# Kernel optimization log

Measured on AMD Instinct MI355X. Metric: run time of the kernel, lower is better.

## Reference

```python
import jax, jax.numpy as jnp
import numpy as np

HEADS, LEVELS, POINTS, DIMS = 8, 4, 4, 256
CH = DIMS // HEADS
SHAPES = np.array([[96, 96], [48, 48], [24, 24], [12, 12]], dtype=np.int64)
LEVEL_START = np.concatenate([[0], np.cumsum(SHAPES[:, 0] * SHAPES[:, 1])[:-1]]).astype(np.int64)
HW = int((SHAPES[:, 0] * SHAPES[:, 1]).sum())
N, Q = 2, HW


def setup_inputs() -> dict:
    key = jax.random.key(0)
    ks = jax.random.split(key, 8)
    return {
        "q": jax.random.normal(ks[0], (N, Q, DIMS), jnp.float32),
        "p": jax.random.uniform(ks[1], (N, Q, LEVELS, 2), jnp.float32),
        "v": jax.random.normal(ks[2], (N, HW, DIMS), jnp.float32),
        "W_off": jax.random.normal(ks[3], (DIMS, HEADS * LEVELS * POINTS * 2), jnp.float32) * 0.01,
        "b_off": jax.random.normal(ks[4], (HEADS * LEVELS * POINTS * 2,), jnp.float32) * 0.5,
        "W_attn": jax.random.normal(ks[5], (DIMS, HEADS * LEVELS * POINTS), jnp.float32) * 0.02,
        "b_attn": jnp.zeros((HEADS * LEVELS * POINTS,), jnp.float32),
        "W_in": jax.random.normal(ks[6], (DIMS, DIMS), jnp.float32) / np.float32(np.sqrt(DIMS)),
        "b_in": jnp.zeros((DIMS,), jnp.float32),
        "W_out": jax.random.normal(ks[7], (DIMS, DIMS), jnp.float32) / np.float32(np.sqrt(DIMS)),
        "b_out": jnp.zeros((DIMS,), jnp.float32),
        "shapes": jnp.asarray(SHAPES),
        "level_index": jnp.asarray(LEVEL_START),
    }


def _sample_level(vl, loc_l, Hl, Wl):
    """Bilinear sample with zero padding outside the feature map.
    vl: [N, Hl*Wl, heads, C]; loc_l: [N, Q, heads, P, 2] normalized (x, y) in [0,1].
    Returns [N, Q, P, heads, C]."""
    Nb, Qn, Hd, P, _ = loc_l.shape
    x = loc_l[..., 0] * Wl - 0.5  # pixel coords, align_corners=False convention
    y = loc_l[..., 1] * Hl - 0.5
    x0 = jnp.floor(x)
    y0 = jnp.floor(y)
    dx = x - x0
    dy = y - y0
    x0i = x0.astype(jnp.int32)
    y0i = y0.astype(jnp.int32)
    out = jnp.zeros((Nb, Qn, P, Hd, vl.shape[-1]), vl.dtype)
    corners = ((x0i, y0i, (1 - dx) * (1 - dy)), (x0i + 1, y0i, dx * (1 - dy)),
               (x0i, y0i + 1, (1 - dx) * dy), (x0i + 1, y0i + 1, dx * dy))
    for cx, cy, w in corners:
        valid = (cx >= 0) & (cx < Wl) & (cy >= 0) & (cy < Hl)
        idx = jnp.clip(cy, 0, Hl - 1) * Wl + jnp.clip(cx, 0, Wl - 1)  # [N,Q,Hd,P]
        idx_t = idx.transpose(0, 1, 3, 2).reshape(Nb, Qn * P, Hd, 1)
        g = jnp.take_along_axis(vl, idx_t, axis=1).reshape(Nb, Qn, P, Hd, -1)
        wv = jnp.where(valid, w, 0.0).transpose(0, 1, 3, 2)  # [N,Q,P,Hd]
        out = out + g * wv[..., None].astype(vl.dtype)
    return out


def _forward(q, p, v, W_off, b_off, W_attn, b_attn, W_in, b_in, W_out, b_out, shp, lsi):
    Nb, Qn, _ = q.shape
    v = (v @ W_in + b_in).reshape(Nb, -1, HEADS, CH)
    off = (q @ W_off + b_off).reshape(Nb, Qn, HEADS, LEVELS, POINTS, 2)
    attn = jax.nn.softmax((q @ W_attn + b_attn).reshape(Nb, Qn, HEADS, LEVELS * POINTS), axis=-1)
    attn = attn.reshape(Nb, Qn, HEADS, LEVELS, POINTS)
    # offsets normalized by (W, H) of each level, added to reference points (2-coord branch)
    off_norm = jnp.asarray(np.stack([shp[:, 1], shp[:, 0]], -1), q.dtype)  # [L, 2]
    loc = p[:, :, None, :, None, :] + off / off_norm[None, None, None, :, None, :]  # [N,Q,Hd,L,P,2]
    out = jnp.zeros((Nb, Qn, HEADS, CH), q.dtype)
    for l in range(LEVELS):
        Hl, Wl = int(shp[l, 0]), int(shp[l, 1])
        s = int(lsi[l])
        vl = jax.lax.slice_in_dim(v, s, s + Hl * Wl, axis=1)
        samp = _sample_level(vl, loc[:, :, :, l], Hl, Wl)  # [N,Q,P,Hd,C]
        out = out + jnp.einsum('nqphc,nqhp->nqhc', samp, attn[:, :, :, l])
    return out.reshape(Nb, Qn, DIMS) @ W_out + b_out


def reference(q, p, v, W_off, b_off, W_attn, b_attn, W_in, b_in, W_out, b_out, shapes, level_index):
    shp = np.asarray(shapes)  # spatial shapes are structural constants
    lsi = np.asarray(level_index)
    return _forward(q, p, v, W_off, b_off, W_attn, b_attn, W_in, b_in, W_out, b_out, shp, lsi)
```

## Files before the change

kernel.cpp:

```cpp
#include <hip/hip_runtime.h>
#include <hip/hip_bf16.h>
#include <math.h>

#define NB      2
#define QN      12240
#define HW_TOT  12240
#define DIMS    256
#define HEADS   8
#define CH      32
#define LEVELS  4
#define POINTS  4
#define M_TOT   (NB * QN)

typedef unsigned short ushort_t;
typedef __attribute__((ext_vector_type(8))) short short8;
typedef __attribute__((ext_vector_type(4))) float floatx4;

__device__ __constant__ int c_Hl[4]    = {96, 48, 24, 12};
__device__ __constant__ int c_Wl[4]    = {96, 48, 24, 12};
__device__ __constant__ int c_start[4] = {0, 9216, 11520, 12096};

__device__ __forceinline__ ushort_t f2bf(float f) {
    __hip_bfloat16 h = __float2bfloat16(f);
    return *reinterpret_cast<ushort_t*>(&h);
}

__global__ __launch_bounds__(256) void convert_qv_kernel(
    const float* __restrict__ v, const float* __restrict__ q,
    ushort_t* __restrict__ vbf, ushort_t* __restrict__ qbf)
{
    const size_t i = ((size_t)blockIdx.x * 256 + threadIdx.x) * 8;
    const size_t half = (size_t)M_TOT * DIMS;
    const float* src; ushort_t* dst; size_t off;
    if (i < half) { src = v; dst = vbf; off = i; }
    else          { src = q; dst = qbf; off = i - half; }
    const float4 a = *(const float4*)&src[off];
    const float4 b = *(const float4*)&src[off + 4];
    ushort_t t[8] = {f2bf(a.x), f2bf(a.y), f2bf(a.z), f2bf(a.w),
                     f2bf(b.x), f2bf(b.y), f2bf(b.z), f2bf(b.w)};
    *(int4*)&dst[off] = *(int4*)t;
}

__global__ __launch_bounds__(256) void prep_weights_kernel(
    const float* __restrict__ W_in, const float* __restrict__ W_off,
    const float* __restrict__ W_attn, const float* __restrict__ W_out,
    const float* __restrict__ b_off, const float* __restrict__ b_attn,
    ushort_t* __restrict__ Tin, ushort_t* __restrict__ Tcomb,
    ushort_t* __restrict__ Tout, float* __restrict__ bcomb)
{
    const int z  = blockIdx.z;
    const int gi = blockIdx.x * 256 + threadIdx.x;
    if (z == 1 && gi < 384)
        bcomb[gi] = (gi < 256) ? b_off[gi] : b_attn[gi - 256];
    const int Nw = (z == 1) ? 384 : 256;
    if (gi >= Nw * 256) return;
    const int k = gi & 255;
    const int n = gi >> 8;
    float val; ushort_t* T;
    if (z == 0)      { val = W_in[k * 256 + n];  T = Tin;  }
    else if (z == 1) { val = (n < 256) ? W_off[k * 256 + n]
                                       : W_attn[k * 128 + (n - 256)]; T = Tcomb; }
    else             { val = W_out[k * 256 + n]; T = Tout; }
    T[n * 256 + k] = f2bf(val);
}

__device__ __forceinline__ void gemm_tile_core(
    const ushort_t* __restrict__ A, const ushort_t* __restrict__ BT,
    const float* __restrict__ bias, void* __restrict__ C, bool c_bf16,
    int M, int Nc, int bm0, int bn0, int K,
    ushort_t* As, ushort_t* Bs)
{
    const int tid  = threadIdx.x;
    const int wave = tid >> 6;
    const int lane = tid & 63;
    const int quad = lane >> 4;
    const int l16  = lane & 15;
    const int wm   = (wave >> 1) * 64;
    const int wn   = (wave & 1) * 64;

    const int off0 = tid * 16;
    const int row0 = off0 >> 6;
    const int kc0  = (off0 & 63) >> 1;

    int ar0 = bm0 + row0;      if (ar0 > M - 1) ar0 = M - 1;
    int ar1 = bm0 + row0 + 64; if (ar1 > M - 1) ar1 = M - 1;

    const ushort_t* ga0 = A  + (size_t)ar0 * K + kc0;
    const ushort_t* ga1 = A  + (size_t)ar1 * K + kc0;
    const ushort_t* gb0 = BT + (size_t)(bn0 + row0) * K + kc0;
    const ushort_t* gb1 = BT + (size_t)(bn0 + row0 + 64) * K + kc0;

    ushort_t* lA0 = As + wave * 512;
    ushort_t* lA1 = As + wave * 512 + 2048;
    ushort_t* lB0 = Bs + wave * 512;
    ushort_t* lB1 = Bs + wave * 512 + 2048;

    floatx4 acc[4][4];
    #pragma unroll
    for (int i = 0; i < 4; ++i)
        #pragma unroll
        for (int j = 0; j < 4; ++j)
            acc[i][j] = (floatx4){0.f, 0.f, 0.f, 0.f};

    for (int kk = 0; kk < K; kk += 32) {
        __builtin_amdgcn_global_load_lds(
            (const __attribute__((address_space(1))) void*)(ga0 + kk),
            (__attribute__((address_space(3))) void*)lA0, 16, 0, 0);
        __builtin_amdgcn_global_load_lds(
            (const __attribute__((address_space(1))) void*)(ga1 + kk),
            (__attribute__((address_space(3))) void*)lA1, 16, 0, 0);
        __builtin_amdgcn_global_load_lds(
            (const __attribute__((address_space(1))) void*)(gb0 + kk),
            (__attribute__((address_space(3))) void*)lB0, 16, 0, 0);
        __builtin_amdgcn_global_load_lds(
            (const __attribute__((address_space(1))) void*)(gb1 + kk),
            (__attribute__((address_space(3))) void*)lB1, 16, 0, 0);
        __syncthreads();

        short8 af[4], bfr[4];
        #pragma unroll
        for (int mt = 0; mt < 4; ++mt)
            af[mt] = *(const short8*)&As[(wm + mt * 16 + l16) * 32 + quad * 8];
        #pragma unroll
        for (int nt = 0; nt < 4; ++nt)
            bfr[nt] = *(const short8*)&Bs[(wn + nt * 16 + l16) * 32 + quad * 8];
        #pragma unroll
        for (int mt = 0; mt < 4; ++mt)
            #pragma unroll
            for (int nt = 0; nt < 4; ++nt)
                acc[mt][nt] = __builtin_amdgcn_mfma_f32_16x16x32_bf16(
                    af[mt], bfr[nt], acc[mt][nt], 0, 0, 0);
        __syncthreads();
    }

    #pragma unroll
    for (int mt = 0; mt < 4; ++mt) {
        #pragma unroll
        for (int j = 0; j < 4; ++j) {
            const int row = bm0 + wm + mt * 16 + quad * 4 + j;
            if (row >= M) continue;
            #pragma unroll
            for (int nt = 0; nt < 4; ++nt) {
                const int col = bn0 + wn + nt * 16 + l16;
                const float val = acc[mt][nt][j] + bias[col];
                if (c_bf16) ((ushort_t*)C)[(size_t)row * Nc + col] = f2bf(val);
                else        ((float*)C)[(size_t)row * Nc + col]    = val;
            }
        }
    }
}

__global__ __launch_bounds__(256) void gemm_proj_kernel(
    const ushort_t* __restrict__ vbf, const ushort_t* __restrict__ qbf,
    const ushort_t* __restrict__ Tin, const ushort_t* __restrict__ Tcomb,
    const float* __restrict__ b_in, const float* __restrict__ bcomb,
    ushort_t* __restrict__ vproj, float* __restrict__ offlog)
{
    __shared__ ushort_t As[128 * 32];
    __shared__ ushort_t Bs[128 * 32];
    const int bm0 = blockIdx.x * 128;
    const int y = blockIdx.y;
    if (y < 2)
        gemm_tile_core(vbf, Tin, b_in, vproj, true, M_TOT, 256, bm0, y * 128, 256, As, Bs);
    else
        gemm_tile_core(qbf, Tcomb, bcomb, offlog, false, M_TOT, 384, bm0, (y - 2) * 128, 256, As, Bs);
}

__global__ __launch_bounds__(256) void gemm_out_kernel(
    const ushort_t* __restrict__ mid, const ushort_t* __restrict__ Tout,
    const float* __restrict__ b_out, float* __restrict__ out)
{
    __shared__ ushort_t As[128 * 32];
    __shared__ ushort_t Bs[128 * 32];
    gemm_tile_core(mid, Tout, b_out, out, false, M_TOT, 256,
                   blockIdx.x * 128, blockIdx.y * 128, 256, As, Bs);
}

#define QB 2
#define SLOTS 576

__global__ __launch_bounds__(128) void msda_sample_kernel(
    const ushort_t* __restrict__ vproj, const float* __restrict__ offlog,
    const float* __restrict__ p, ushort_t* __restrict__ mid)
{
    __shared__ float s_logit[QB][128];
    __shared__ float s_off[QB][256];
    __shared__ float s_p[QB][8];
    __shared__ float s_mx[QB][HEADS];
    __shared__ float s_inv[QB][HEADS];
    __shared__ float s_w[QB][SLOTS];
    __shared__ int   s_idx[QB][SLOTS];

    const int tid = threadIdx.x;
    const int bq0 = blockIdx.x * QB;

    #pragma unroll
    for (int i = tid; i < QB * 256; i += 128) {
        int sub = i >> 8, j = i & 255;
        s_off[sub][j] = offlog[(size_t)(bq0 + sub) * 384 + j];
    }
    #pragma unroll
    for (int i = tid; i < QB * 128; i += 128) {
        int sub = i >> 7, j = i & 127;
        s_logit[sub][j] = offlog[(size_t)(bq0 + sub) * 384 + 256 + j];
    }
    if (tid < QB * 8) {
        int sub = tid >> 3, j = tid & 7;
        s_p[sub][j] = p[(size_t)(bq0 + sub) * 8 + j];
    }
    __syncthreads();

    if (tid < QB * HEADS) {
        int sub = tid >> 3, h = tid & 7;
        float mx = -1e30f;
        #pragma unroll
        for (int i = 0; i < 16; ++i) mx = fmaxf(mx, s_logit[sub][h * 16 + i]);
        float ssum = 0.0f;
        #pragma unroll
        for (int i = 0; i < 16; ++i) ssum += __expf(s_logit[sub][h * 16 + i] - mx);
        s_mx[sub][h] = mx;
        s_inv[sub][h] = 1.0f / ssum;
    }
    __syncthreads();

    #pragma unroll
    for (int tt = tid; tt < QB * 128; tt += 128) {
        const int sub = tt >> 7;
        const int j   = tt & 127;
        const int h   = j >> 4;
        const int l   = (j >> 2) & 3;
        const int nq  = bq0 + sub;
        const int nb  = (nq >= QN) ? 1 : 0;

        const int Hl = c_Hl[l], Wl = c_Wl[l], st = c_start[l];
        const float fW = (float)Wl, fH = (float)Hl;

        const float w = __expf(s_logit[sub][j] - s_mx[sub][h]) * s_inv[sub][h];

        const int oi = j * 2;
        const float ox = s_off[sub][oi];
        const float oy = s_off[sub][oi + 1];
        const float px = s_p[sub][l * 2 + 0];
        const float py = s_p[sub][l * 2 + 1];

        const float lx = px + ox / fW;
        const float ly = py + oy / fH;
        const float x = lx * fW - 0.5f;
        const float y = ly * fH - 0.5f;

        const float x0f = floorf(x), y0f = floorf(y);
        const int x0 = (int)x0f, y0 = (int)y0f;
        const float dx = x - x0f, dy = y - y0f;

        const int base = nb * (HW_TOT * DIMS) + h * CH;
        const int slot = (j & 15) * 36 + h * 4;

        const bool vx0 = (x0 >= 0) & (x0 < Wl);
        const bool vx1 = (x0 + 1 >= 0) & (x0 + 1 < Wl);
        const bool vy0 = (y0 >= 0) & (y0 < Hl);
        const bool vy1 = (y0 + 1 >= 0) & (y0 + 1 < Hl);

        s_w[sub][slot + 0] = (vx0 & vy0) ? w * (1.0f - dx) * (1.0f - dy) : 0.0f;
        s_w[sub][slot + 1] = (vx1 & vy0) ? w * dx * (1.0f - dy) : 0.0f;
        s_w[sub][slot + 2] = (vx0 & vy1) ? w * (1.0f - dx) * dy : 0.0f;
        s_w[sub][slot + 3] = (vx1 & vy1) ? w * dx * dy : 0.0f;
        s_idx[sub][slot + 0] = (vx0 & vy0) ? base + (st + y0 * Wl + x0) * DIMS : 0;
        s_idx[sub][slot + 1] = (vx1 & vy0) ? base + (st + y0 * Wl + x0 + 1) * DIMS : 0;
        s_idx[sub][slot + 2] = (vx0 & vy1) ? base + (st + (y0 + 1) * Wl + x0) * DIMS : 0;
        s_idx[sub][slot + 3] = (vx1 & vy1) ? base + (st + (y0 + 1) * Wl + x0 + 1) * DIMS : 0;
    }
    __syncthreads();

    const int sub  = tid >> 6;
    const int lane = tid & 63;
    const int h    = lane >> 3;
    const int c4   = lane & 7;
    const int nq   = bq0 + sub;

    float ax = 0.0f, ay = 0.0f, az = 0.0f, aw = 0.0f;
    const ushort_t* __restrict__ vb = vproj + c4 * 4;

    #pragma unroll
    for (int t = 0; t < 16; ++t) {
        const int slot = t * 36 + h * 4;
        const int4   I = *(const int4*)&s_idx[sub][slot];
        const float4 W = *(const float4*)&s_w[sub][slot];

        const uint2 g0 = *(const uint2*)(vb + I.x);
        const uint2 g1 = *(const uint2*)(vb + I.y);
        const uint2 g2 = *(const uint2*)(vb + I.z);
        const uint2 g3 = *(const uint2*)(vb + I.w);

        ax = fmaf(W.x, __uint_as_float(g0.x << 16), ax);
        ay = fmaf(W.x, __uint_as_float(g0.x & 0xffff0000u), ay);
        az = fmaf(W.x, __uint_as_float(g0.y << 16), az);
        aw = fmaf(W.x, __uint_as_float(g0.y & 0xffff0000u), aw);

        ax = fmaf(W.y, __uint_as_float(g1.x << 16), ax);
        ay = fmaf(W.y, __uint_as_float(g1.x & 0xffff0000u), ay);
        az = fmaf(W.y, __uint_as_float(g1.y << 16), az);
        aw = fmaf(W.y, __uint_as_float(g1.y & 0xffff0000u), aw);

        ax = fmaf(W.z, __uint_as_float(g2.x << 16), ax);
        ay = fmaf(W.z, __uint_as_float(g2.x & 0xffff0000u), ay);
        az = fmaf(W.z, __uint_as_float(g2.y << 16), az);
        aw = fmaf(W.z, __uint_as_float(g2.y & 0xffff0000u), aw);

        ax = fmaf(W.w, __uint_as_float(g3.x << 16), ax);
        ay = fmaf(W.w, __uint_as_float(g3.x & 0xffff0000u), ay);
        az = fmaf(W.w, __uint_as_float(g3.y << 16), az);
        aw = fmaf(W.w, __uint_as_float(g3.y & 0xffff0000u), aw);
    }

    ushort_t mv[4] = {f2bf(ax), f2bf(ay), f2bf(az), f2bf(aw)};
    *(uint2*)&mid[(size_t)nq * DIMS + lane * 4] = *(uint2*)mv;
}

extern "C" void kernel_launch(void* const* d_in, const int* in_sizes, int n_in,
                              void* d_out, int out_size, void* d_ws, size_t ws_size,
                              hipStream_t stream)
{
    const float* q      = (const float*)d_in[0];
    const float* p      = (const float*)d_in[1];
    const float* v      = (const float*)d_in[2];
    const float* W_off  = (const float*)d_in[3];
    const float* b_off  = (const float*)d_in[4];
    const float* W_attn = (const float*)d_in[5];
    const float* b_attn = (const float*)d_in[6];
    const float* W_in   = (const float*)d_in[7];
    const float* b_in   = (const float*)d_in[8];
    const float* W_out  = (const float*)d_in[9];
    const float* b_out  = (const float*)d_in[10];
    float* out = (float*)d_out;

    const int M = M_TOT;

    ushort_t* vproj  = (ushort_t*)d_ws;
    float*    offlog = (float*)(vproj + (size_t)M * 256);
    ushort_t* vbf    = (ushort_t*)(offlog + (size_t)M * 384);
    ushort_t* mid    = vbf;
    ushort_t* qbf    = vbf + (size_t)M * 256;
    ushort_t* Tin    = qbf + (size_t)M * 256;
    ushort_t* Tcomb  = Tin + 256 * 256;
    ushort_t* Tout   = Tcomb + 384 * 256;
    float*    bcomb  = (float*)(Tout + 256 * 256);

    convert_qv_kernel<<<dim3(6120), 256, 0, stream>>>(v, q, vbf, qbf);
    prep_weights_kernel<<<dim3(384, 1, 3), 256, 0, stream>>>(
        W_in, W_off, W_attn, W_out, b_off, b_attn, Tin, Tcomb, Tout, bcomb);

    gemm_proj_kernel<<<dim3(192, 5), 256, 0, stream>>>(
        vbf, qbf, Tin, Tcomb, b_in, bcomb, vproj, offlog);
    msda_sample_kernel<<<dim3(M / QB), 128, 0, stream>>>(vproj, offlog, p, mid);
    gemm_out_kernel<<<dim3(192, 2), 256, 0, stream>>>(mid, Tout, b_out, out);
}
```

Before: 208.6 us.

## Load GEMM fragments directly from global and widen sampler gathers to 16 bytes

The GEMM core no longer stages A/B tiles through LDS with global_load_lds and barriers. Each wave now reads its MFMA fragments straight from global memory, relying on cache for reuse, with K fixed at 256 and the epilogue output type as a template parameter. Separately, the sampling kernel drops to 64 threads per block, and each lane gathers 8 bf16 channels (uint4) per corner instead of 4. This means fewer, wider gather loads and less per-block overhead, at the cost of redundant global reads in the GEMM and lower parallelism in the sampler.

```diff
diff --git a/kernel.cpp b/kernel.cpp
--- a/kernel.cpp
+++ b/kernel.cpp
@@ -64,11 +64,11 @@
     T[n * 256 + k] = f2bf(val);
 }
 
-__device__ __forceinline__ void gemm_tile_core(
+template<bool C_BF16>
+__device__ __forceinline__ void gemm_direct(
     const ushort_t* __restrict__ A, const ushort_t* __restrict__ BT,
-    const float* __restrict__ bias, void* __restrict__ C, bool c_bf16,
-    int M, int Nc, int bm0, int bn0, int K,
-    ushort_t* As, ushort_t* Bs)
+    const float* __restrict__ bias, void* __restrict__ Cv,
+    int M, int Nc, int bm0, int bn0)
 {
     const int tid  = threadIdx.x;
     const int wave = tid >> 6;
@@ -78,22 +78,17 @@
     const int wm   = (wave >> 1) * 64;
     const int wn   = (wave & 1) * 64;
 
-    const int off0 = tid * 16;
-    const int row0 = off0 >> 6;
-    const int kc0  = (off0 & 63) >> 1;
-
-    int ar0 = bm0 + row0;      if (ar0 > M - 1) ar0 = M - 1;
-    int ar1 = bm0 + row0 + 64; if (ar1 > M - 1) ar1 = M - 1;
-
-    const ushort_t* ga0 = A  + (size_t)ar0 * K + kc0;
-    const ushort_t* ga1 = A  + (size_t)ar1 * K + kc0;
-    const ushort_t* gb0 = BT + (size_t)(bn0 + row0) * K + kc0;
-    const ushort_t* gb1 = BT + (size_t)(bn0 + row0 + 64) * K + kc0;
-
-    ushort_t* lA0 = As + wave * 512;
-    ushort_t* lA1 = As + wave * 512 + 2048;
-    ushort_t* lB0 = Bs + wave * 512;
-    ushort_t* lB1 = Bs + wave * 512 + 2048;
+    const ushort_t* ap[4];
+    const ushort_t* bp[4];
+    #pragma unroll
+    for (int mt = 0; mt < 4; ++mt) {
+        int r = bm0 + wm + mt * 16 + l16;
+        if (r > M - 1) r = M - 1;
+        ap[mt] = A + (size_t)r * 256 + quad * 8;
+    }
+    #pragma unroll
+    for (int nt = 0; nt < 4; ++nt)
+        bp[nt] = BT + (size_t)(bn0 + wn + nt * 16 + l16) * 256 + quad * 8;
 
     floatx4 acc[4][4];
     #pragma unroll
@@ -102,35 +97,19 @@
         for (int j = 0; j < 4; ++j)
             acc[i][j] = (floatx4){0.f, 0.f, 0.f, 0.f};
 
-    for (int kk = 0; kk < K; kk += 32) {
-        __builtin_amdgcn_global_load_lds(
-            (const __attribute__((address_space(1))) void*)(ga0 + kk),
-            (__attribute__((address_space(3))) void*)lA0, 16, 0, 0);
-        __builtin_amdgcn_global_load_lds(
-            (const __attribute__((address_space(1))) void*)(ga1 + kk),
-            (__attribute__((address_space(3))) void*)lA1, 16, 0, 0);
-        __builtin_amdgcn_global_load_lds(
-            (const __attribute__((address_space(1))) void*)(gb0 + kk),
-            (__attribute__((address_space(3))) void*)lB0, 16, 0, 0);
-        __builtin_amdgcn_global_load_lds(
-            (const __attribute__((address_space(1))) void*)(gb1 + kk),
-            (__attribute__((address_space(3))) void*)lB1, 16, 0, 0);
-        __syncthreads();
-
+    #pragma unroll
+    for (int kk = 0; kk < 256; kk += 32) {
         short8 af[4], bfr[4];
         #pragma unroll
-        for (int mt = 0; mt < 4; ++mt)
-            af[mt] = *(const short8*)&As[(wm + mt * 16 + l16) * 32 + quad * 8];
-        #pragma unroll
-        for (int nt = 0; nt < 4; ++nt)
-            bfr[nt] = *(const short8*)&Bs[(wn + nt * 16 + l16) * 32 + quad * 8];
+        for (int mt = 0; mt < 4; ++mt) af[mt]  = *(const short8*)(ap[mt] + kk);
+        #pragma unroll
+        for (int nt = 0; nt < 4; ++nt) bfr[nt] = *(const short8*)(bp[nt] + kk);
         #pragma unroll
         for (int mt = 0; mt < 4; ++mt)
             #pragma unroll
             for (int nt = 0; nt < 4; ++nt)
                 acc[mt][nt] = __builtin_amdgcn_mfma_f32_16x16x32_bf16(
                     af[mt], bfr[nt], acc[mt][nt], 0, 0, 0);
-        __syncthreads();
     }
 
     #pragma unroll
@@ -143,8 +122,8 @@
             for (int nt = 0; nt < 4; ++nt) {
                 const int col = bn0 + wn + nt * 16 + l16;
                 const float val = acc[mt][nt][j] + bias[col];
-                if (c_bf16) ((ushort_t*)C)[(size_t)row * Nc + col] = f2bf(val);
-                else        ((float*)C)[(size_t)row * Nc + col]    = val;
+                if (C_BF16) ((ushort_t*)Cv)[(size_t)row * Nc + col] = f2bf(val);
+                else        ((float*)Cv)[(size_t)row * Nc + col]    = val;
             }
         }
     }
@@ -156,30 +135,26 @@
     const float* __restrict__ b_in, const float* __restrict__ bcomb,
     ushort_t* __restrict__ vproj, float* __restrict__ offlog)
 {
-    __shared__ ushort_t As[128 * 32];
-    __shared__ ushort_t Bs[128 * 32];
     const int bm0 = blockIdx.x * 128;
     const int y = blockIdx.y;
     if (y < 2)
-        gemm_tile_core(vbf, Tin, b_in, vproj, true, M_TOT, 256, bm0, y * 128, 256, As, Bs);
+        gemm_direct<true>(vbf, Tin, b_in, vproj, M_TOT, 256, bm0, y * 128);
     else
-        gemm_tile_core(qbf, Tcomb, bcomb, offlog, false, M_TOT, 384, bm0, (y - 2) * 128, 256, As, Bs);
+        gemm_direct<false>(qbf, Tcomb, bcomb, offlog, M_TOT, 384, bm0, (y - 2) * 128);
 }
 
 __global__ __launch_bounds__(256) void gemm_out_kernel(
     const ushort_t* __restrict__ mid, const ushort_t* __restrict__ Tout,
     const float* __restrict__ b_out, float* __restrict__ out)
 {
-    __shared__ ushort_t As[128 * 32];
-    __shared__ ushort_t Bs[128 * 32];
-    gemm_tile_core(mid, Tout, b_out, out, false, M_TOT, 256,
-                   blockIdx.x * 128, blockIdx.y * 128, 256, As, Bs);
+    gemm_direct<false>(mid, Tout, b_out, out, M_TOT, 256,
+                       blockIdx.x * 128, blockIdx.y * 128);
 }
 
 #define QB 2
 #define SLOTS 576
 
-__global__ __launch_bounds__(128) void msda_sample_kernel(
+__global__ __launch_bounds__(64) void msda_sample_kernel(
     const ushort_t* __restrict__ vproj, const float* __restrict__ offlog,
     const float* __restrict__ p, ushort_t* __restrict__ mid)
 {
@@ -195,12 +170,12 @@
     const int bq0 = blockIdx.x * QB;
 
     #pragma unroll
-    for (int i = tid; i < QB * 256; i += 128) {
+    for (int i = tid; i < QB * 256; i += 64) {
         int sub = i >> 8, j = i & 255;
         s_off[sub][j] = offlog[(size_t)(bq0 + sub) * 384 + j];
     }
     #pragma unroll
-    for (int i = tid; i < QB * 128; i += 128) {
+    for (int i = tid; i < QB * 128; i += 64) {
         int sub = i >> 7, j = i & 127;
         s_logit[sub][j] = offlog[(size_t)(bq0 + sub) * 384 + 256 + j];
     }
@@ -224,7 +199,7 @@
     __syncthreads();
 
     #pragma unroll
-    for (int tt = tid; tt < QB * 128; tt += 128) {
+    for (int tt = tid; tt < QB * 128; tt += 64) {
         const int sub = tt >> 7;
         const int j   = tt & 127;
         const int h   = j >> 4;
@@ -271,14 +246,14 @@
     }
     __syncthreads();
 
-    const int sub  = tid >> 6;
-    const int lane = tid & 63;
-    const int h    = lane >> 3;
-    const int c4   = lane & 7;
-    const int nq   = bq0 + sub;
-
-    float ax = 0.0f, ay = 0.0f, az = 0.0f, aw = 0.0f;
-    const ushort_t* __restrict__ vb = vproj + c4 * 4;
+    const int sub    = tid >> 5;
+    const int lane32 = tid & 31;
+    const int h      = lane32 >> 2;
+    const int c16    = lane32 & 3;
+    const int nq     = bq0 + sub;
+
+    float a0=0.f,a1=0.f,a2=0.f,a3=0.f,a4=0.f,a5=0.f,a6=0.f,a7=0.f;
+    const ushort_t* __restrict__ vb = vproj + c16 * 8;
 
     #pragma unroll
     for (int t = 0; t < 16; ++t) {
@@ -286,34 +261,51 @@
         const int4   I = *(const int4*)&s_idx[sub][slot];
         const float4 W = *(const float4*)&s_w[sub][slot];
 
-        const uint2 g0 = *(const uint2*)(vb + I.x);
-        const uint2 g1 = *(const uint2*)(vb + I.y);
-        const uint2 g2 = *(const uint2*)(vb + I.z);
-        const uint2 g3 = *(const uint2*)(vb + I.w);
-
-        ax = fmaf(W.x, __uint_as_float(g0.x << 16), ax);
-        ay = fmaf(W.x, __uint_as_float(g0.x & 0xffff0000u), ay);
-        az = fmaf(W.x, __uint_as_float(g0.y << 16), az);
-        aw = fmaf(W.x, __uint_as_float(g0.y & 0xffff0000u), aw);
-
-        ax = fmaf(W.y, __uint_as_float(g1.x << 16), ax);
-        ay = fmaf(W.y, __uint_as_float(g1.x & 0xffff0000u), ay);
-        az = fmaf(W.y, __uint_as_float(g1.y << 16), az);
-        aw = fmaf(W.y, __uint_as_float(g1.y & 0xffff0000u), aw);
-
-        ax = fmaf(W.z, __uint_as_float(g2.x << 16), ax);
-        ay = fmaf(W.z, __uint_as_float(g2.x & 0xffff0000u), ay);
-        az = fmaf(W.z, __uint_as_float(g2.y << 16), az);
-        aw = fmaf(W.z, __uint_as_float(g2.y & 0xffff0000u), aw);
-
-        ax = fmaf(W.w, __uint_as_float(g3.x << 16), ax);
-        ay = fmaf(W.w, __uint_as_float(g3.x & 0xffff0000u), ay);
-        az = fmaf(W.w, __uint_as_float(g3.y << 16), az);
-        aw = fmaf(W.w, __uint_as_float(g3.y & 0xffff0000u), aw);
-    }
-
-    ushort_t mv[4] = {f2bf(ax), f2bf(ay), f2bf(az), f2bf(aw)};
-    *(uint2*)&mid[(size_t)nq * DIMS + lane * 4] = *(uint2*)mv;
+        const uint4 g0 = *(const uint4*)(vb + I.x);
+        const uint4 g1 = *(const uint4*)(vb + I.y);
+        const uint4 g2 = *(const uint4*)(vb + I.z);
+        const uint4 g3 = *(const uint4*)(vb + I.w);
+
+        a0 = fmaf(W.x, __uint_as_float(g0.x << 16), a0);
+        a1 = fmaf(W.x, __uint_as_float(g0.x & 0xffff0000u), a1);
+        a2 = fmaf(W.x, __uint_as_float(g0.y << 16), a2);
+        a3 = fmaf(W.x, __uint_as_float(g0.y & 0xffff0000u), a3);
+        a4 = fmaf(W.x, __uint_as_float(g0.z << 16), a4);
+        a5 = fmaf(W.x, __uint_as_float(g0.z & 0xffff0000u), a5);
+        a6 = fmaf(W.x, __uint_as_float(g0.w << 16), a6);
+        a7 = fmaf(W.x, __uint_as_float(g0.w & 0xffff0000u), a7);
+
+        a0 = fmaf(W.y, __uint_as_float(g1.x << 16), a0);
+        a1 = fmaf(W.y, __uint_as_float(g1.x & 0xffff0000u), a1);
+        a2 = fmaf(W.y, __uint_as_float(g1.y << 16), a2);
+        a3 = fmaf(W.y, __uint_as_float(g1.y & 0xffff0000u), a3);
+        a4 = fmaf(W.y, __uint_as_float(g1.z << 16), a4);
+        a5 = fmaf(W.y, __uint_as_float(g1.z & 0xffff0000u), a5);
+        a6 = fmaf(W.y, __uint_as_float(g1.w << 16), a6);
+        a7 = fmaf(W.y, __uint_as_float(g1.w & 0xffff0000u), a7);
+
+        a0 = fmaf(W.z, __uint_as_float(g2.x << 16), a0);
+        a1 = fmaf(W.z, __uint_as_float(g2.x & 0xffff0000u), a1);
+        a2 = fmaf(W.z, __uint_as_float(g2.y << 16), a2);
+        a3 = fmaf(W.z, __uint_as_float(g2.y & 0xffff0000u), a3);
+        a4 = fmaf(W.z, __uint_as_float(g2.z << 16), a4);
+        a5 = fmaf(W.z, __uint_as_float(g2.z & 0xffff0000u), a5);
+        a6 = fmaf(W.z, __uint_as_float(g2.w << 16), a6);
+        a7 = fmaf(W.z, __uint_as_float(g2.w & 0xffff0000u), a7);
+
+        a0 = fmaf(W.w, __uint_as_float(g3.x << 16), a0);
+        a1 = fmaf(W.w, __uint_as_float(g3.x & 0xffff0000u), a1);
+        a2 = fmaf(W.w, __uint_as_float(g3.y << 16), a2);
+        a3 = fmaf(W.w, __uint_as_float(g3.y & 0xffff0000u), a3);
+        a4 = fmaf(W.w, __uint_as_float(g3.z << 16), a4);
+        a5 = fmaf(W.w, __uint_as_float(g3.z & 0xffff0000u), a5);
+        a6 = fmaf(W.w, __uint_as_float(g3.w << 16), a6);
+        a7 = fmaf(W.w, __uint_as_float(g3.w & 0xffff0000u), a7);
+    }
+
+    ushort_t mv[8] = {f2bf(a0), f2bf(a1), f2bf(a2), f2bf(a3),
+                      f2bf(a4), f2bf(a5), f2bf(a6), f2bf(a7)};
+    *(int4*)&mid[(size_t)nq * DIMS + h * CH + c16 * 8] = *(int4*)mv;
 }
 
 extern "C" void kernel_launch(void* const* d_in, const int* in_sizes, int n_in,
@@ -351,6 +343,6 @@
 
     gemm_proj_kernel<<<dim3(192, 5), 256, 0, stream>>>(
         vbf, qbf, Tin, Tcomb, b_in, bcomb, vproj, offlog);
-    msda_sample_kernel<<<dim3(M / QB), 128, 0, stream>>>(vproj, offlog, p, mid);
+    msda_sample_kernel<<<dim3(M / QB), 64, 0, stream>>>(vproj, offlog, p, mid);
     gemm_out_kernel<<<dim3(192, 2), 256, 0, stream>>>(mid, Tout, b_out, out);
 }
```

Result: slower. 328.5 us (+57.4%).
